# Kernel optimization log

Measured on AMD Instinct MI355X. Metric: run time of the kernel, lower is better.

Reference implementation:

```python
import jax, jax.numpy as jnp
import numpy as np

N_NODES = 100000
N_EDGES = 1600000
D_IN, D_HID, D_OUT = 64, 64, 2


def setup_inputs() -> dict:
    key = jax.random.key(0)
    k1, k2, k3, k4 = jax.random.split(key, 4)
    x = jax.random.normal(k1, (N_NODES, D_IN), dtype=jnp.float32)
    edge_index = jax.random.randint(k2, (2, N_EDGES), 0, N_NODES, dtype=jnp.int64)
    W1 = jax.random.normal(k3, (D_IN, D_HID), dtype=jnp.float32) * (1.0 / np.sqrt(D_IN))
    b1 = jnp.zeros((D_HID,), dtype=jnp.float32)
    W2 = jax.random.normal(k4, (D_HID, D_OUT), dtype=jnp.float32) * (1.0 / np.sqrt(D_HID))
    b2 = jnp.zeros((D_OUT,), dtype=jnp.float32)
    return {"x": x, "edge_index": edge_index, "W1": W1, "b1": b1, "W2": W2, "b2": b2}


def _gcn_norm(edge_index, num_nodes):
    # PyG GCNConv default: add self-loops, symmetric normalization D^-1/2 (A+I) D^-1/2
    loops = jnp.arange(num_nodes, dtype=edge_index.dtype)
    row = jnp.concatenate([edge_index[0], loops])  # source
    col = jnp.concatenate([edge_index[1], loops])  # destination
    deg = jax.ops.segment_sum(jnp.ones_like(col, dtype=jnp.float32), col, num_segments=num_nodes)
    dinv = jnp.where(deg > 0, jax.lax.rsqrt(deg), 0.0)
    norm = dinv[row] * dinv[col]  # [E + N]
    return row, col, norm


def _gcn_conv(x, W, b, row, col, norm, num_nodes):
    h = x @ W                              # [N, D_out] small GEMM first (PyG order)
    msg = h[row] * norm[:, None]           # gather + scale  [E+N, D_out]
    out = jax.ops.segment_sum(msg, col, num_segments=num_nodes)  # scatter-add
    return out + b


def reference(x, edge_index, W1, b1, W2, b2):
    n = x.shape[0]
    row, col, norm = _gcn_norm(edge_index, n)
    h = jax.nn.relu(_gcn_conv(x, W1, b1, row, col, norm, n))
    return _gcn_conv(h, W2, b2, row, col, norm, n)
```

## Files before the change

kernel.cpp:

```cpp
#include <hip/hip_runtime.h>


#define D_IN 64
#define NBBITS 10
#define NBK_PAD 128
#define BSTRIDE 16
#define PCH 8192
#define BCAP 16384
#define BCAPE 24576

__device__ __forceinline__ float b2f(unsigned short u) {
    unsigned v = ((unsigned)u) << 16;
    float f;
    __builtin_memcpy(&f, &v, 4);
    return f;
}
__device__ __forceinline__ unsigned short f2b(float f) {
    unsigned u;
    __builtin_memcpy(&u, &f, 4);
    u += 0x7FFFu + ((u >> 16) & 1u);
    return (unsigned short)(u >> 16);
}

__device__ __forceinline__ int edge_val(const int* __restrict__ p, int f64, long pos) {
    return f64 ? p[2 * pos] : p[pos];
}

__device__ __forceinline__ void acc8(float* a, uint4 rv, float wgt) {
    a[0] = fmaf(wgt, b2f((unsigned short)(rv.x & 0xFFFFu)), a[0]);
    a[1] = fmaf(wgt, b2f((unsigned short)(rv.x >> 16)), a[1]);
    a[2] = fmaf(wgt, b2f((unsigned short)(rv.y & 0xFFFFu)), a[2]);
    a[3] = fmaf(wgt, b2f((unsigned short)(rv.y >> 16)), a[3]);
    a[4] = fmaf(wgt, b2f((unsigned short)(rv.z & 0xFFFFu)), a[4]);
    a[5] = fmaf(wgt, b2f((unsigned short)(rv.z >> 16)), a[5]);
    a[6] = fmaf(wgt, b2f((unsigned short)(rv.w & 0xFFFFu)), a[6]);
    a[7] = fmaf(wgt, b2f((unsigned short)(rv.w >> 16)), a[7]);
}

__global__ __launch_bounds__(1024, 8) void k_part_gemm(
        const int* __restrict__ ep, int* __restrict__ bptr,
        unsigned* __restrict__ ebuf,
        const float* __restrict__ x, const float* __restrict__ W,
        unsigned short* __restrict__ H, int E, int N, int nPart) {
    __shared__ __align__(16) char smraw[51200];
    int tid = threadIdx.x;
    int lane = tid & 63;

    if (blockIdx.x < nPart) {
        int* hist  = (int*)smraw;
        int* lofs  = hist + NBK_PAD;
        int* gbase = lofs + NBK_PAD;
        int* fsh   = gbase + NBK_PAD;
        unsigned* stage = (unsigned*)(fsh + 4);

        if (tid < NBK_PAD) hist[tid] = 0;
        if (tid < 64) {
            int bad = 0;
            for (int i = tid; i < 1024; i += 64)
                if (ep[2 * i + 1] != 0) bad = 1;
            unsigned long long m = __ballot(bad);
            if (tid == 0) fsh[0] = (m == 0ull) ? 1 : 0;
        }
        __syncthreads();
        int f = fsh[0];
        long base = (long)blockIdx.x * PCH;
        long rem64 = (long)E - base;
        int nE = rem64 > PCH ? PCH : (int)rem64;
        int j0 = tid * 8;
        int nv = nE - j0;
        nv = nv < 0 ? 0 : (nv > 8 ? 8 : nv);
        unsigned cc[8], rr2[8];
        #pragma unroll
        for (int k = 0; k < 8; ++k) { cc[k] = 0; rr2[k] = 0; }
        bool fullv = (nv == 8);
        const uint4* p4 = (const uint4*)ep;
        if (f) {
            if (fullv && ((E & 1) == 0)) {
                size_t cb = ((size_t)E + (size_t)base + j0) >> 1;
                uint4 a0 = p4[cb + 0], a1 = p4[cb + 1];
                uint4 a2 = p4[cb + 2], a3 = p4[cb + 3];
                cc[0] = a0.x; cc[1] = a0.z; cc[2] = a1.x; cc[3] = a1.z;
                cc[4] = a2.x; cc[5] = a2.z; cc[6] = a3.x; cc[7] = a3.z;
            } else {
                for (int k = 0; k < 8; ++k)
                    if (k < nv) cc[k] = (unsigned)ep[2 * ((size_t)E + base + j0 + k)];
            }
        } else {
            if (fullv && ((E & 3) == 0)) {
                size_t cb = ((size_t)E + (size_t)base + j0) >> 2;
                uint4 a0 = p4[cb + 0], a1 = p4[cb + 1];
                cc[0] = a0.x; cc[1] = a0.y; cc[2] = a0.z; cc[3] = a0.w;
                cc[4] = a1.x; cc[5] = a1.y; cc[6] = a1.z; cc[7] = a1.w;
            } else {
                for (int k = 0; k < 8; ++k)
                    if (k < nv) cc[k] = (unsigned)ep[(size_t)E + base + j0 + k];
            }
        }
        #pragma unroll
        for (int k = 0; k < 8; ++k)
            if (k < nv) atomicAdd(&hist[cc[k] >> NBBITS], 1);
        if (f) {
            if (fullv && ((E & 1) == 0)) {
                size_t rb = ((size_t)base + j0) >> 1;
                uint4 b0 = p4[rb + 0], b1 = p4[rb + 1];
                uint4 b2 = p4[rb + 2], b3 = p4[rb + 3];
                rr2[0] = b0.x; rr2[1] = b0.z; rr2[2] = b1.x; rr2[3] = b1.z;
                rr2[4] = b2.x; rr2[5] = b2.z; rr2[6] = b3.x; rr2[7] = b3.z;
            } else {
                for (int k = 0; k < 8; ++k)
                    if (k < nv) rr2[k] = (unsigned)ep[2 * ((size_t)base + j0 + k)];
            }
        } else {
            if (fullv && ((E & 3) == 0)) {
                size_t rb = ((size_t)base + j0) >> 2;
                uint4 b0 = p4[rb + 0], b1 = p4[rb + 1];
                rr2[0] = b0.x; rr2[1] = b0.y; rr2[2] = b0.z; rr2[3] = b0.w;
                rr2[4] = b1.x; rr2[5] = b1.y; rr2[6] = b1.z; rr2[7] = b1.w;
            } else {
                for (int k = 0; k < 8; ++k)
                    if (k < nv) rr2[k] = (unsigned)ep[(size_t)base + j0 + k];
            }
        }
        __syncthreads();
        if (tid < NBK_PAD) {
            int c = hist[tid], s = c;
            #pragma unroll
            for (int off = 1; off < 64; off <<= 1) {
                int t2 = __shfl(s, lane - off);
                if (lane >= off) s += t2;
            }
            if (lane == 63) fsh[1 + (tid >> 6)] = s;
            lofs[tid] = s - c;
        }
        __syncthreads();
        if (tid >= 64 && tid < NBK_PAD) lofs[tid] += fsh[1];
        if (tid < NBK_PAD) hist[tid] = 0;
        __syncthreads();
        #pragma unroll
        for (int k = 0; k < 8; ++k) {
            if (k < nv) {
                unsigned c = cc[k];
                int b = c >> NBBITS;
                int pos = lofs[b] + atomicAdd(&hist[b], 1);
                stage[pos] = rr2[k] | ((c & ((1u << NBBITS) - 1)) << 17);
            }
        }
        __syncthreads();
        if (tid < NBK_PAD && hist[tid])
            gbase[tid] = atomicAdd(&bptr[tid * BSTRIDE], hist[tid]);
        __syncthreads();
        int wv = tid >> 6;
        for (int b = wv; b < NBK_PAD; b += 16) {
            int c = hist[b];
            if (c == 0) continue;
            int lo = lofs[b], go = gbase[b];
            unsigned* dst = ebuf + (size_t)b * BCAPE + go;
            for (int j = lane; j < c; j += 64) dst[j] = stage[lo + j];
        }
    } else {
        float* Ws = (float*)smraw;
        float* Xs = (float*)(smraw + 16384);
        int wv = tid >> 6;
        for (int i = tid; i < 64 * 64; i += 1024) Ws[i] = W[i];

        int bid = blockIdx.x - nPart;
        int ngb = gridDim.x - nPart;
        int ntiles = (N + 127) >> 7;
        for (int tile = bid; tile < ntiles; tile += ngb) {
            int rr = tid >> 4, c4 = tid & 15;
            int g0 = (tile << 7) + rr;
            int g1 = g0 + 64;
            float4 v0 = make_float4(0.f, 0.f, 0.f, 0.f);
            float4 v1 = make_float4(0.f, 0.f, 0.f, 0.f);
            if (g0 < N) v0 = *(const float4*)(x + (size_t)g0 * 64 + c4 * 4);
            if (g1 < N) v1 = *(const float4*)(x + (size_t)g1 * 64 + c4 * 4);
            __syncthreads();
            *(float4*)(&Xs[rr * 68 + c4 * 4]) = v0;
            *(float4*)(&Xs[(rr + 64) * 68 + c4 * 4]) = v1;
            __syncthreads();
            float acc[8];
            #pragma unroll
            for (int r = 0; r < 8; ++r) acc[r] = 0.f;
            int rbase = wv * 8;
            #pragma unroll 4
            for (int k4 = 0; k4 < 16; ++k4) {
                float w0 = Ws[(4 * k4 + 0) * 64 + lane];
                float w1 = Ws[(4 * k4 + 1) * 64 + lane];
                float w2 = Ws[(4 * k4 + 2) * 64 + lane];
                float w3 = Ws[(4 * k4 + 3) * 64 + lane];
                #pragma unroll
                for (int r = 0; r < 8; ++r) {
                    float4 xq = *(const float4*)(&Xs[(rbase + r) * 68 + k4 * 4]);
                    acc[r] = fmaf(xq.x, w0, acc[r]);
                    acc[r] = fmaf(xq.y, w1, acc[r]);
                    acc[r] = fmaf(xq.z, w2, acc[r]);
                    acc[r] = fmaf(xq.w, w3, acc[r]);
                }
            }
            int row0 = (tile << 7) + rbase;
            #pragma unroll
            for (int r = 0; r < 8; ++r) {
                int row = row0 + r;
                if (row < N) H[(size_t)row * 64 + lane] = f2b(acc[r]);
            }
        }
    }
}

__global__ __launch_bounds__(1024) void k_bucket(const unsigned* __restrict__ ebuf,
                                                 const int* __restrict__ bptr,
                                                 int* __restrict__ offs,
                                                 float* __restrict__ dinv,
                                                 int* __restrict__ srcA, int N, int E) {
    __shared__ int hist[1024], escan[1024], wsum[16];
    __shared__ int bco[NBK_PAD];
    __shared__ int stage[BCAP];
    int tid = threadIdx.x, b = blockIdx.x;
    int lane = tid & 63, wid = tid >> 6;
    hist[tid] = 0;
    if (tid < NBK_PAD) {
        int c = bptr[tid * BSTRIDE];
        int s = c;
        #pragma unroll
        for (int off = 1; off < 64; off <<= 1) {
            int t = __shfl(s, lane - off);
            if (lane >= off) s += t;
        }
        if (lane == 63) wsum[wid] = s;
        bco[tid] = s - c;
    }
    if (tid == 0 && b == 0) offs[N] = E;
    __syncthreads();
    if (tid >= 64 && tid < NBK_PAD) bco[tid] += wsum[0];
    __syncthreads();

    int rbase = b * BCAPE;
    int lo = bco[b];
    int m = bptr[b * BSTRIDE];
    for (int i = tid; i < m; i += 1024) {
        unsigned w = ebuf[rbase + i];
        atomicAdd(&hist[w >> 17], 1);
    }
    __syncthreads();
    int v = hist[tid];
    int s = v;
    #pragma unroll
    for (int off = 1; off < 64; off <<= 1) {
        int t = __shfl(s, lane - off);
        if (lane >= off) s += t;
    }
    if (lane == 63) wsum[wid] = s;
    __syncthreads();
    if (tid < 16) {
        int xv = wsum[tid];
        int ss = xv;
        #pragma unroll
        for (int off = 1; off < 16; off <<= 1) {
            int t = __shfl(ss, lane - off);
            if (lane >= off) ss += t;
        }
        wsum[tid] = ss - xv;
    }
    __syncthreads();
    int excl = s - v + wsum[wid];
    escan[tid] = excl;
    int g = (b << NBBITS) + tid;
    if (g < N) {
        offs[g] = lo + excl;
        dinv[g] = rsqrtf((float)(v + 1));
    }
    __syncthreads();
    for (int i = tid; i < m; i += 1024) {
        unsigned w = ebuf[rbase + i];
        int lc = w >> 17;
        int src = (int)(w & 0x1FFFFu);
        int sl = escan[lc] + atomicSub(&hist[lc], 1) - 1;
        if (sl < BCAP) stage[sl] = src;
        else srcA[lo + sl] = src;
    }
    __syncthreads();
    int mm = min(m, BCAP);
    for (int i = tid; i < mm; i += 1024) srcA[lo + i] = stage[i];
}

__global__ void k_agg1(const unsigned short* __restrict__ H1,
                       const int* __restrict__ srcA,
                       const float* __restrict__ dinv, const int* __restrict__ offs,
                       const float* __restrict__ b1, const float* __restrict__ W2,
                       float* __restrict__ Z, int N) {
    int wid = (blockIdx.x * blockDim.x + threadIdx.x) >> 6;
    int lane = threadIdx.x & 63;
    int g = lane >> 3, s = lane & 7;
    int n = wid * 8 + g;
    bool nvalid = (n < N);
    int nn = nvalid ? n : 0;
    float dn = dinv[nn];
    int base = offs[nn];
    int cnt = nvalid ? (offs[nn + 1] - base) : 0;
    int cm = cnt;
    #pragma unroll
    for (int off = 8; off <= 32; off <<= 1) cm = max(cm, __shfl_xor(cm, off));
    const uint4* H4 = (const uint4*)H1;
    uint4 rs = H4[(size_t)nn * 8 + s];
    float4 b1a = *(const float4*)(b1 + s * 8);
    float4 b1b = *(const float4*)(b1 + s * 8 + 4);
    const float4* w2p = (const float4*)(W2 + s * 16);
    float4 q0 = w2p[0], q1 = w2p[1], q2 = w2p[2], q3 = w2p[3];
    float a[8];
    #pragma unroll
    for (int k = 0; k < 8; ++k) a[k] = 0.f;
    int gb = g << 3;
    int sv = 0; float wl = 0.f;
    if (s < cnt) { sv = srcA[base + s]; wl = dinv[sv]; }
    for (int j0 = 0; j0 < cm; j0 += 8) {
        int svn = 0; float wln = 0.f;
        int jn = j0 + 8;
        if (jn + s < cnt) { svn = srcA[base + jn + s]; wln = dinv[svn]; }
        int   s0 = __shfl(sv, gb + 0), s1 = __shfl(sv, gb + 1);
        int   s2 = __shfl(sv, gb + 2), s3 = __shfl(sv, gb + 3);
        int   s4 = __shfl(sv, gb + 4), s5 = __shfl(sv, gb + 5);
        int   s6 = __shfl(sv, gb + 6), s7 = __shfl(sv, gb + 7);
        float w0 = __shfl(wl, gb + 0), w1 = __shfl(wl, gb + 1);
        float w2 = __shfl(wl, gb + 2), w3 = __shfl(wl, gb + 3);
        float w4 = __shfl(wl, gb + 4), w5 = __shfl(wl, gb + 5);
        float w6 = __shfl(wl, gb + 6), w7 = __shfl(wl, gb + 7);
        uint4 r0 = H4[(size_t)s0 * 8 + s];
        uint4 r1 = H4[(size_t)s1 * 8 + s];
        uint4 r2 = H4[(size_t)s2 * 8 + s];
        uint4 r3 = H4[(size_t)s3 * 8 + s];
        uint4 r4 = H4[(size_t)s4 * 8 + s];
        uint4 r5 = H4[(size_t)s5 * 8 + s];
        uint4 r6 = H4[(size_t)s6 * 8 + s];
        uint4 r7 = H4[(size_t)s7 * 8 + s];
        acc8(a, r0, w0); acc8(a, r1, w1); acc8(a, r2, w2); acc8(a, r3, w3);
        acc8(a, r4, w4); acc8(a, r5, w5); acc8(a, r6, w6); acc8(a, r7, w7);
        sv = svn; wl = wln;
    }
    acc8(a, rs, dn);
    float h0 = fmaxf(dn * a[0] + b1a.x, 0.f);
    float h1 = fmaxf(dn * a[1] + b1a.y, 0.f);
    float h2 = fmaxf(dn * a[2] + b1a.z, 0.f);
    float h3 = fmaxf(dn * a[3] + b1a.w, 0.f);
    float h4 = fmaxf(dn * a[4] + b1b.x, 0.f);
    float h5 = fmaxf(dn * a[5] + b1b.y, 0.f);
    float h6 = fmaxf(dn * a[6] + b1b.z, 0.f);
    float h7 = fmaxf(dn * a[7] + b1b.w, 0.f);
    float p0 = h0 * q0.x + h1 * q0.z + h2 * q1.x + h3 * q1.z
             + h4 * q2.x + h5 * q2.z + h6 * q3.x + h7 * q3.z;
    float p1 = h0 * q0.y + h1 * q0.w + h2 * q1.y + h3 * q1.w
             + h4 * q2.y + h5 * q2.w + h6 * q3.y + h7 * q3.w;
    #pragma unroll
    for (int off = 1; off < 8; off <<= 1) {
        p0 += __shfl_xor(p0, off);
        p1 += __shfl_xor(p1, off);
    }
    if (s == 0 && nvalid) { Z[n * 2 + 0] = p0; Z[n * 2 + 1] = p1; }
}

__global__ void k_agg2(const float* __restrict__ Z, const int* __restrict__ srcA,
                       const float* __restrict__ dinv, const int* __restrict__ offs,
                       const float* __restrict__ b2, float* __restrict__ out, int N) {
    int t = blockIdx.x * blockDim.x + threadIdx.x;
    int lane = threadIdx.x & 63;
    int n = (t >> 6) * 4 + (lane >> 4);
    int sl = lane & 15;
    if (n >= N) return;
    int base = offs[n];
    int cnt = offs[n + 1] - base;
    float a0 = 0.f, a1 = 0.f;
    const float2* Z2 = (const float2*)Z;
    for (int i = sl; i < cnt; i += 16) {
        int src = srcA[base + i];
        float w = dinv[src];
        float2 zv = Z2[src];
        a0 += w * zv.x;
        a1 += w * zv.y;
    }
    #pragma unroll
    for (int off = 8; off > 0; off >>= 1) {
        a0 += __shfl_xor(a0, off);
        a1 += __shfl_xor(a1, off);
    }
    if (sl == 0) {
        float dn = dinv[n];
        float2 zs = Z2[n];
        out[n * 2 + 0] = dn * (a0 + dn * zs.x) + b2[0];
        out[n * 2 + 1] = dn * (a1 + dn * zs.y) + b2[1];
    }
}

extern "C" void kernel_launch(void* const* d_in, const int* in_sizes, int n_in,
                              void* d_out, int out_size, void* d_ws, size_t ws_size,
                              hipStream_t stream) {
    const float* x  = (const float*)d_in[0];
    const int*   ep = (const int*)d_in[1];
    const float* W1 = (const float*)d_in[2];
    const float* b1 = (const float*)d_in[3];
    const float* W2 = (const float*)d_in[4];
    const float* b2 = (const float*)d_in[5];
    float* out = (float*)d_out;

    const int N = in_sizes[0] / D_IN;
    const int E = in_sizes[1] / 2;

    char* ws = (char*)d_ws;
    size_t o = 0;
    auto alloc = [&](size_t bytes) {
        size_t r = o;
        o = (o + bytes + 255) & ~(size_t)255;
        return r;
    };
    int*            bptr  = (int*)           (ws + alloc((size_t)NBK_PAD * BSTRIDE * 4));
    float*          dinv  = (float*)         (ws + alloc((size_t)N * 4));
    int*            offs  = (int*)           (ws + alloc((size_t)(N + 1) * 4));
    unsigned*       ebuf  = (unsigned*)      (ws + alloc((size_t)NBK_PAD * BCAPE * 4));
    int*            srcA  = (int*)           (ws + alloc((size_t)E * 4));
    unsigned short* H1    = (unsigned short*)(ws + alloc((size_t)N * 64 * 2));
    float*          Z     = (float*)         (ws + alloc((size_t)N * 2 * 4));

    const int nbk = (N + (1 << NBBITS) - 1) >> NBBITS;
    const int nPart = (E + PCH - 1) / PCH;
    int nGemm = 512 - nPart;
    if (nGemm < 64) nGemm = 64;

    (void)hipMemsetAsync(bptr, 0, (size_t)NBK_PAD * BSTRIDE * sizeof(int), stream);
    k_part_gemm<<<nPart + nGemm, 1024, 0, stream>>>(ep, bptr, ebuf, x, W1, H1, E, N, nPart);
    k_bucket<<<nbk, 1024, 0, stream>>>(ebuf, bptr, offs, dinv, srcA, N, E);
    int nwav = (N + 7) / 8;
    k_agg1<<<(nwav + 3) / 4, 256, 0, stream>>>(H1, srcA, dinv, offs, b1, W2, Z, N);
    k_agg2<<<(N + 15) / 16, 256, 0, stream>>>(Z, srcA, dinv, offs, b2, out, N);
}
```

Baseline: 104.6 us.

## Fuse bucket sort with layer-1 aggregation using finer buckets and global degree counts

Buckets shrink from 1024 to 256 destination nodes, giving 512 buckets, and the per-bucket CSR build is merged with the first aggregation kernel. Each block now sorts its bucket's edges and aggregates its nodes directly from shared-memory staged sources, which removes one kernel launch and a global round trip for srcA. Source-node normalisation needs degrees of nodes in other buckets, so the partition kernel now keeps a global per-node degree array via atomics. This adds 1.6M global atomics and an rsqrt per edge, and leaves only 4 small blocks of nodes per 1024-thread block for aggregation work, which may limit parallelism.

After: 164.7 us. 1.57x slower.

```diff
diff --git a/kernel.cpp b/kernel.cpp
--- a/kernel.cpp
+++ b/kernel.cpp
@@ -2,12 +2,11 @@
 
 
 #define D_IN 64
-#define NBBITS 10
-#define NBK_PAD 128
+#define NBBITS 8
+#define NBK_PAD 512
 #define BSTRIDE 16
 #define PCH 8192
-#define BCAP 16384
-#define BCAPE 24576
+#define SCAP 5120
 
 __device__ __forceinline__ float b2f(unsigned short u) {
     unsigned v = ((unsigned)u) << 16;
@@ -20,10 +19,6 @@
     __builtin_memcpy(&u, &f, 4);
     u += 0x7FFFu + ((u >> 16) & 1u);
     return (unsigned short)(u >> 16);
-}
-
-__device__ __forceinline__ int edge_val(const int* __restrict__ p, int f64, long pos) {
-    return f64 ? p[2 * pos] : p[pos];
 }
 
 __device__ __forceinline__ void acc8(float* a, uint4 rv, float wgt) {
@@ -39,7 +34,7 @@
 
 __global__ __launch_bounds__(1024, 8) void k_part_gemm(
         const int* __restrict__ ep, int* __restrict__ bptr,
-        unsigned* __restrict__ ebuf,
+        int* __restrict__ deg, unsigned* __restrict__ ebuf,
         const float* __restrict__ x, const float* __restrict__ W,
         unsigned short* __restrict__ H, int E, int N, int nPart) {
     __shared__ __align__(16) char smraw[51200];
@@ -51,7 +46,7 @@
         int* lofs  = hist + NBK_PAD;
         int* gbase = lofs + NBK_PAD;
         int* fsh   = gbase + NBK_PAD;
-        unsigned* stage = (unsigned*)(fsh + 4);
+        unsigned* stage = (unsigned*)(fsh + 16);
 
         if (tid < NBK_PAD) hist[tid] = 0;
         if (tid < 64) {
@@ -98,12 +93,15 @@
         }
         #pragma unroll
         for (int k = 0; k < 8; ++k)
-            if (k < nv) atomicAdd(&hist[cc[k] >> NBBITS], 1);
+            if (k < nv) {
+                atomicAdd(&hist[cc[k] >> NBBITS], 1);
+                atomicAdd(&deg[cc[k]], 1);
+            }
         if (f) {
             if (fullv && ((E & 1) == 0)) {
-                size_t rb = ((size_t)base + j0) >> 1;
-                uint4 b0 = p4[rb + 0], b1 = p4[rb + 1];
-                uint4 b2 = p4[rb + 2], b3 = p4[rb + 3];
+                size_t rbb = ((size_t)base + j0) >> 1;
+                uint4 b0 = p4[rbb + 0], b1 = p4[rbb + 1];
+                uint4 b2 = p4[rbb + 2], b3 = p4[rbb + 3];
                 rr2[0] = b0.x; rr2[1] = b0.z; rr2[2] = b1.x; rr2[3] = b1.z;
                 rr2[4] = b2.x; rr2[5] = b2.z; rr2[6] = b3.x; rr2[7] = b3.z;
             } else {
@@ -112,8 +110,8 @@
             }
         } else {
             if (fullv && ((E & 3) == 0)) {
-                size_t rb = ((size_t)base + j0) >> 2;
-                uint4 b0 = p4[rb + 0], b1 = p4[rb + 1];
+                size_t rbb = ((size_t)base + j0) >> 2;
+                uint4 b0 = p4[rbb + 0], b1 = p4[rbb + 1];
                 rr2[0] = b0.x; rr2[1] = b0.y; rr2[2] = b0.z; rr2[3] = b0.w;
                 rr2[4] = b1.x; rr2[5] = b1.y; rr2[6] = b1.z; rr2[7] = b1.w;
             } else {
@@ -133,16 +131,22 @@
             lofs[tid] = s - c;
         }
         __syncthreads();
-        if (tid >= 64 && tid < NBK_PAD) lofs[tid] += fsh[1];
-        if (tid < NBK_PAD) hist[tid] = 0;
+        if (tid < NBK_PAD) {
+            int w8 = tid >> 6, add = 0;
+            #pragma unroll
+            for (int q = 0; q < 8; ++q)
+                if (q < w8) add += fsh[1 + q];
+            lofs[tid] += add;
+            hist[tid] = 0;
+        }
         __syncthreads();
         #pragma unroll
         for (int k = 0; k < 8; ++k) {
             if (k < nv) {
                 unsigned c = cc[k];
-                int b = c >> NBBITS;
-                int pos = lofs[b] + atomicAdd(&hist[b], 1);
-                stage[pos] = rr2[k] | ((c & ((1u << NBBITS) - 1)) << 17);
+                int bb = c >> NBBITS;
+                int pos = lofs[bb] + atomicAdd(&hist[bb], 1);
+                stage[pos] = rr2[k] | ((c & 255u) << 17);
             }
         }
         __syncthreads();
@@ -150,12 +154,12 @@
             gbase[tid] = atomicAdd(&bptr[tid * BSTRIDE], hist[tid]);
         __syncthreads();
         int wv = tid >> 6;
-        for (int b = wv; b < NBK_PAD; b += 16) {
-            int c = hist[b];
+        for (int bb = wv; bb < NBK_PAD; bb += 16) {
+            int c = hist[bb];
             if (c == 0) continue;
-            int lo = lofs[b], go = gbase[b];
-            unsigned* dst = ebuf + (size_t)b * BCAPE + go;
-            for (int j = lane; j < c; j += 64) dst[j] = stage[lo + j];
+            int lo2 = lofs[bb], go = gbase[bb];
+            unsigned* dst = ebuf + (size_t)bb * SCAP + go;
+            for (int j = lane; j < c; j += 64) dst[j] = stage[lo2 + j];
         }
     } else {
         float* Ws = (float*)smraw;
@@ -207,154 +211,145 @@
     }
 }
 
-__global__ __launch_bounds__(1024) void k_bucket(const unsigned* __restrict__ ebuf,
-                                                 const int* __restrict__ bptr,
-                                                 int* __restrict__ offs,
-                                                 float* __restrict__ dinv,
-                                                 int* __restrict__ srcA, int N, int E) {
-    __shared__ int hist[1024], escan[1024], wsum[16];
-    __shared__ int bco[NBK_PAD];
-    __shared__ int stage[BCAP];
+__global__ __launch_bounds__(1024, 4) void k_bucket_agg(
+        const unsigned* __restrict__ ebuf, const int* __restrict__ bptr,
+        const int* __restrict__ deg,
+        int* __restrict__ offs, float* __restrict__ dinv,
+        int* __restrict__ srcA,
+        const unsigned short* __restrict__ H1,
+        const float* __restrict__ b1, const float* __restrict__ W2,
+        float* __restrict__ Z, int N, int E) {
+    __shared__ int cntS[256];
+    __shared__ int escan[257];
+    __shared__ float dinvsh[256];
+    __shared__ int wsum[16];
+    __shared__ int loSh;
+    __shared__ int stage[SCAP];
     int tid = threadIdx.x, b = blockIdx.x;
     int lane = tid & 63, wid = tid >> 6;
-    hist[tid] = 0;
-    if (tid < NBK_PAD) {
-        int c = bptr[tid * BSTRIDE];
-        int s = c;
-        #pragma unroll
-        for (int off = 1; off < 64; off <<= 1) {
-            int t = __shfl(s, lane - off);
-            if (lane >= off) s += t;
-        }
-        if (lane == 63) wsum[wid] = s;
-        bco[tid] = s - c;
-    }
-    if (tid == 0 && b == 0) offs[N] = E;
-    __syncthreads();
-    if (tid >= 64 && tid < NBK_PAD) bco[tid] += wsum[0];
-    __syncthreads();
-
-    int rbase = b * BCAPE;
-    int lo = bco[b];
-    int m = bptr[b * BSTRIDE];
-    for (int i = tid; i < m; i += 1024) {
-        unsigned w = ebuf[rbase + i];
-        atomicAdd(&hist[w >> 17], 1);
-    }
-    __syncthreads();
-    int v = hist[tid];
-    int s = v;
-    #pragma unroll
-    for (int off = 1; off < 64; off <<= 1) {
-        int t = __shfl(s, lane - off);
-        if (lane >= off) s += t;
-    }
-    if (lane == 63) wsum[wid] = s;
-    __syncthreads();
-    if (tid < 16) {
-        int xv = wsum[tid];
-        int ss = xv;
-        #pragma unroll
-        for (int off = 1; off < 16; off <<= 1) {
-            int t = __shfl(ss, lane - off);
-            if (lane >= off) ss += t;
-        }
-        wsum[tid] = ss - xv;
-    }
-    __syncthreads();
-    int excl = s - v + wsum[wid];
-    escan[tid] = excl;
-    int g = (b << NBBITS) + tid;
-    if (g < N) {
-        offs[g] = lo + excl;
-        dinv[g] = rsqrtf((float)(v + 1));
-    }
-    __syncthreads();
-    for (int i = tid; i < m; i += 1024) {
-        unsigned w = ebuf[rbase + i];
-        int lc = w >> 17;
-        int src = (int)(w & 0x1FFFFu);
-        int sl = escan[lc] + atomicSub(&hist[lc], 1) - 1;
-        if (sl < BCAP) stage[sl] = src;
-        else srcA[lo + sl] = src;
-    }
-    __syncthreads();
-    int mm = min(m, BCAP);
-    for (int i = tid; i < mm; i += 1024) srcA[lo + i] = stage[i];
-}
-
-__global__ void k_agg1(const unsigned short* __restrict__ H1,
-                       const int* __restrict__ srcA,
-                       const float* __restrict__ dinv, const int* __restrict__ offs,
-                       const float* __restrict__ b1, const float* __restrict__ W2,
-                       float* __restrict__ Z, int N) {
-    int wid = (blockIdx.x * blockDim.x + threadIdx.x) >> 6;
-    int lane = threadIdx.x & 63;
-    int g = lane >> 3, s = lane & 7;
-    int n = wid * 8 + g;
-    bool nvalid = (n < N);
-    int nn = nvalid ? n : 0;
-    float dn = dinv[nn];
-    int base = offs[nn];
-    int cnt = nvalid ? (offs[nn + 1] - base) : 0;
-    int cm = cnt;
-    #pragma unroll
-    for (int off = 8; off <= 32; off <<= 1) cm = max(cm, __shfl_xor(cm, off));
-    const uint4* H4 = (const uint4*)H1;
-    uint4 rs = H4[(size_t)nn * 8 + s];
+    int s = tid & 7, gb = lane & 56;
     float4 b1a = *(const float4*)(b1 + s * 8);
     float4 b1b = *(const float4*)(b1 + s * 8 + 4);
     const float4* w2p = (const float4*)(W2 + s * 16);
     float4 q0 = w2p[0], q1 = w2p[1], q2 = w2p[2], q3 = w2p[3];
-    float a[8];
+
+    if (tid < 256) cntS[tid] = 0;
+    int cb = 0;
+    if (tid < NBK_PAD && tid < b) cb = bptr[tid * BSTRIDE];
     #pragma unroll
-    for (int k = 0; k < 8; ++k) a[k] = 0.f;
-    int gb = g << 3;
-    int sv = 0; float wl = 0.f;
-    if (s < cnt) { sv = srcA[base + s]; wl = dinv[sv]; }
-    for (int j0 = 0; j0 < cm; j0 += 8) {
-        int svn = 0; float wln = 0.f;
-        int jn = j0 + 8;
-        if (jn + s < cnt) { svn = srcA[base + jn + s]; wln = dinv[svn]; }
-        int   s0 = __shfl(sv, gb + 0), s1 = __shfl(sv, gb + 1);
-        int   s2 = __shfl(sv, gb + 2), s3 = __shfl(sv, gb + 3);
-        int   s4 = __shfl(sv, gb + 4), s5 = __shfl(sv, gb + 5);
-        int   s6 = __shfl(sv, gb + 6), s7 = __shfl(sv, gb + 7);
-        float w0 = __shfl(wl, gb + 0), w1 = __shfl(wl, gb + 1);
-        float w2 = __shfl(wl, gb + 2), w3 = __shfl(wl, gb + 3);
-        float w4 = __shfl(wl, gb + 4), w5 = __shfl(wl, gb + 5);
-        float w6 = __shfl(wl, gb + 6), w7 = __shfl(wl, gb + 7);
-        uint4 r0 = H4[(size_t)s0 * 8 + s];
-        uint4 r1 = H4[(size_t)s1 * 8 + s];
-        uint4 r2 = H4[(size_t)s2 * 8 + s];
-        uint4 r3 = H4[(size_t)s3 * 8 + s];
-        uint4 r4 = H4[(size_t)s4 * 8 + s];
-        uint4 r5 = H4[(size_t)s5 * 8 + s];
-        uint4 r6 = H4[(size_t)s6 * 8 + s];
-        uint4 r7 = H4[(size_t)s7 * 8 + s];
-        acc8(a, r0, w0); acc8(a, r1, w1); acc8(a, r2, w2); acc8(a, r3, w3);
-        acc8(a, r4, w4); acc8(a, r5, w5); acc8(a, r6, w6); acc8(a, r7, w7);
-        sv = svn; wl = wln;
-    }
-    acc8(a, rs, dn);
-    float h0 = fmaxf(dn * a[0] + b1a.x, 0.f);
-    float h1 = fmaxf(dn * a[1] + b1a.y, 0.f);
-    float h2 = fmaxf(dn * a[2] + b1a.z, 0.f);
-    float h3 = fmaxf(dn * a[3] + b1a.w, 0.f);
-    float h4 = fmaxf(dn * a[4] + b1b.x, 0.f);
-    float h5 = fmaxf(dn * a[5] + b1b.y, 0.f);
-    float h6 = fmaxf(dn * a[6] + b1b.z, 0.f);
-    float h7 = fmaxf(dn * a[7] + b1b.w, 0.f);
-    float p0 = h0 * q0.x + h1 * q0.z + h2 * q1.x + h3 * q1.z
-             + h4 * q2.x + h5 * q2.z + h6 * q3.x + h7 * q3.z;
-    float p1 = h0 * q0.y + h1 * q0.w + h2 * q1.y + h3 * q1.w
-             + h4 * q2.y + h5 * q2.w + h6 * q3.y + h7 * q3.w;
-    #pragma unroll
-    for (int off = 1; off < 8; off <<= 1) {
-        p0 += __shfl_xor(p0, off);
-        p1 += __shfl_xor(p1, off);
-    }
-    if (s == 0 && nvalid) { Z[n * 2 + 0] = p0; Z[n * 2 + 1] = p1; }
+    for (int off = 32; off > 0; off >>= 1) cb += __shfl_xor(cb, off);
+    if (lane == 0) wsum[wid] = cb;
+    __syncthreads();
+    if (tid == 0) {
+        int t = 0;
+        #pragma unroll
+        for (int q = 0; q < 16; ++q) t += wsum[q];
+        loSh = t;
+    }
+    __syncthreads();
+    int lo = loSh;
+    int m = bptr[b * BSTRIDE];
+    size_t rb = (size_t)b * SCAP;
+    for (int i = tid; i < m; i += 1024)
+        atomicAdd(&cntS[ebuf[rb + i] >> 17], 1);
+    __syncthreads();
+    if (tid < 256) {
+        int v = cntS[tid], ss = v;
+        #pragma unroll
+        for (int off = 1; off < 64; off <<= 1) {
+            int t2 = __shfl(ss, lane - off);
+            if (lane >= off) ss += t2;
+        }
+        if (lane == 63) wsum[tid >> 6] = ss;
+        escan[tid] = ss - v;
+    }
+    if (tid == 0) escan[256] = m;
+    __syncthreads();
+    if (tid < 256) {
+        int w4 = tid >> 6, add = 0;
+        #pragma unroll
+        for (int q = 0; q < 4; ++q)
+            if (q < w4) add += wsum[q];
+        int ex = escan[tid] + add;
+        escan[tid] = ex;
+        float dn = rsqrtf((float)(cntS[tid] + 1));
+        dinvsh[tid] = dn;
+        int g = (b << NBBITS) + tid;
+        if (g < N) { offs[g] = lo + ex; dinv[g] = dn; }
+    }
+    if (tid == 0 && b == 0) offs[N] = E;
+    __syncthreads();
+    for (int i = tid; i < m; i += 1024) {
+        unsigned w = ebuf[rb + i];
+        int lc = w >> 17;
+        int src = (int)(w & 0x1FFFFu);
+        int sl = escan[lc] + atomicSub(&cntS[lc], 1) - 1;
+        if (sl < SCAP) stage[sl] = src;
+        else srcA[lo + sl] = src;
+    }
+    __syncthreads();
+    int mm = min(m, SCAP);
+    for (int i = tid; i < mm; i += 1024) srcA[lo + i] = stage[i];
+    const uint4* H4 = (const uint4*)H1;
+    int grp = tid >> 3;
+    for (int r = 0; r < 2; ++r) {
+        int loc = grp + (r << 7);
+        int n = (b << NBBITS) + loc;
+        if (n >= N) break;
+        int start = escan[loc];
+        int cnt = escan[loc + 1] - start;
+        float dn = dinvsh[loc];
+        float a[8];
+        #pragma unroll
+        for (int k = 0; k < 8; ++k) a[k] = 0.f;
+        for (int j = 0; j < cnt; j += 8) {
+            int e = j + s;
+            int sv = 0; float wl = 0.f;
+            if (e < cnt) {
+                int sl = start + e;
+                sv = (sl < SCAP) ? stage[sl] : srcA[lo + sl];
+                wl = rsqrtf((float)(deg[sv] + 1));
+            }
+            int   s0 = __shfl(sv, gb + 0), s1 = __shfl(sv, gb + 1);
+            int   s2 = __shfl(sv, gb + 2), s3 = __shfl(sv, gb + 3);
+            int   s4 = __shfl(sv, gb + 4), s5 = __shfl(sv, gb + 5);
+            int   s6 = __shfl(sv, gb + 6), s7 = __shfl(sv, gb + 7);
+            float w0 = __shfl(wl, gb + 0), w1 = __shfl(wl, gb + 1);
+            float w2 = __shfl(wl, gb + 2), w3 = __shfl(wl, gb + 3);
+            float w4 = __shfl(wl, gb + 4), w5 = __shfl(wl, gb + 5);
+            float w6 = __shfl(wl, gb + 6), w7 = __shfl(wl, gb + 7);
+            uint4 r0 = H4[(size_t)s0 * 8 + s];
+            uint4 r1 = H4[(size_t)s1 * 8 + s];
+            uint4 r2 = H4[(size_t)s2 * 8 + s];
+            uint4 r3 = H4[(size_t)s3 * 8 + s];
+            uint4 r4 = H4[(size_t)s4 * 8 + s];
+            uint4 r5 = H4[(size_t)s5 * 8 + s];
+            uint4 r6 = H4[(size_t)s6 * 8 + s];
+            uint4 r7 = H4[(size_t)s7 * 8 + s];
+            acc8(a, r0, w0); acc8(a, r1, w1); acc8(a, r2, w2); acc8(a, r3, w3);
+            acc8(a, r4, w4); acc8(a, r5, w5); acc8(a, r6, w6); acc8(a, r7, w7);
+        }
+        uint4 rs = H4[(size_t)n * 8 + s];
+        acc8(a, rs, dn);
+        float h0 = fmaxf(dn * a[0] + b1a.x, 0.f);
+        float h1 = fmaxf(dn * a[1] + b1a.y, 0.f);
+        float h2 = fmaxf(dn * a[2] + b1a.z, 0.f);
+        float h3 = fmaxf(dn * a[3] + b1a.w, 0.f);
+        float h4 = fmaxf(dn * a[4] + b1b.x, 0.f);
+        float h5 = fmaxf(dn * a[5] + b1b.y, 0.f);
+        float h6 = fmaxf(dn * a[6] + b1b.z, 0.f);
+        float h7 = fmaxf(dn * a[7] + b1b.w, 0.f);
+        float p0 = h0 * q0.x + h1 * q0.z + h2 * q1.x + h3 * q1.z
+                 + h4 * q2.x + h5 * q2.z + h6 * q3.x + h7 * q3.z;
+        float p1 = h0 * q0.y + h1 * q0.w + h2 * q1.y + h3 * q1.w
+                 + h4 * q2.y + h5 * q2.w + h6 * q3.y + h7 * q3.w;
+        #pragma unroll
+        for (int off = 1; off < 8; off <<= 1) {
+            p0 += __shfl_xor(p0, off);
+            p1 += __shfl_xor(p1, off);
+        }
+        if (s == 0) { Z[n * 2 + 0] = p0; Z[n * 2 + 1] = p1; }
+    }
 }
 
 __global__ void k_agg2(const float* __restrict__ Z, const int* __restrict__ srcA,
@@ -411,9 +406,10 @@
         return r;
     };
     int*            bptr  = (int*)           (ws + alloc((size_t)NBK_PAD * BSTRIDE * 4));
+    int*            deg   = (int*)           (ws + alloc((size_t)N * 4));
     float*          dinv  = (float*)         (ws + alloc((size_t)N * 4));
     int*            offs  = (int*)           (ws + alloc((size_t)(N + 1) * 4));
-    unsigned*       ebuf  = (unsigned*)      (ws + alloc((size_t)NBK_PAD * BCAPE * 4));
+    unsigned*       ebuf  = (unsigned*)      (ws + alloc((size_t)NBK_PAD * SCAP * 4));
     int*            srcA  = (int*)           (ws + alloc((size_t)E * 4));
     unsigned short* H1    = (unsigned short*)(ws + alloc((size_t)N * 64 * 2));
     float*          Z     = (float*)         (ws + alloc((size_t)N * 2 * 4));
@@ -423,10 +419,10 @@
     int nGemm = 512 - nPart;
     if (nGemm < 64) nGemm = 64;
 
-    (void)hipMemsetAsync(bptr, 0, (size_t)NBK_PAD * BSTRIDE * sizeof(int), stream);
-    k_part_gemm<<<nPart + nGemm, 1024, 0, stream>>>(ep, bptr, ebuf, x, W1, H1, E, N, nPart);
-    k_bucket<<<nbk, 1024, 0, stream>>>(ebuf, bptr, offs, dinv, srcA, N, E);
-    int nwav = (N + 7) / 8;
-    k_agg1<<<(nwav + 3) / 4, 256, 0, stream>>>(H1, srcA, dinv, offs, b1, W2, Z, N);
+    (void)hipMemsetAsync(bptr, 0,
+            (size_t)NBK_PAD * BSTRIDE * 4 + (size_t)N * 4, stream);
+    k_part_gemm<<<nPart + nGemm, 1024, 0, stream>>>(ep, bptr, deg, ebuf, x, W1, H1, E, N, nPart);
+    k_bucket_agg<<<nbk, 1024, 0, stream>>>(ebuf, bptr, deg, offs, dinv, srcA,
+                                           H1, b1, W2, Z, N, E);
     k_agg2<<<(N + 15) / 16, 256, 0, stream>>>(Z, srcA, dinv, offs, b2, out, N);
 }
```

## Use bf16 MFMA for first-layer GEMM and per-wave histograms in partitioning

Applied to the files above, without the earlier changes.

The GEMM blocks now convert W to a transposed bf16 tile and compute x@W1 with 16x16x32 bf16 MFMA instructions, one 16-row tile per wave, replacing the scalar FMA loop over shared-memory tiles. The partition blocks switch from a single shared histogram to per-wave histograms with per-wave prefix offsets, which cuts contention on shared-memory atomics during counting and scatter. The grid shrinks from 512 to 256 total blocks and launch bounds drop to 4 blocks per CU. Rounding x to bf16 before the multiply slightly lowers GEMM precision.

New measurement: 97.11 us. -7.1%, faster.

```diff
diff --git a/kernel.cpp b/kernel.cpp
--- a/kernel.cpp
+++ b/kernel.cpp
@@ -9,6 +9,9 @@
 #define BCAP 16384
 #define BCAPE 24576
 
+typedef __attribute__((ext_vector_type(8))) short bf16x8;
+typedef __attribute__((ext_vector_type(4))) float f32x4;
+
 __device__ __forceinline__ float b2f(unsigned short u) {
     unsigned v = ((unsigned)u) << 16;
     float f;
@@ -20,10 +23,6 @@
     __builtin_memcpy(&u, &f, 4);
     u += 0x7FFFu + ((u >> 16) & 1u);
     return (unsigned short)(u >> 16);
-}
-
-__device__ __forceinline__ int edge_val(const int* __restrict__ p, int f64, long pos) {
-    return f64 ? p[2 * pos] : p[pos];
 }
 
 __device__ __forceinline__ void acc8(float* a, uint4 rv, float wgt) {
@@ -37,23 +36,25 @@
     a[7] = fmaf(wgt, b2f((unsigned short)(rv.w >> 16)), a[7]);
 }
 
-__global__ __launch_bounds__(1024, 8) void k_part_gemm(
+__global__ __launch_bounds__(1024, 4) void k_part_gemm(
         const int* __restrict__ ep, int* __restrict__ bptr,
         unsigned* __restrict__ ebuf,
         const float* __restrict__ x, const float* __restrict__ W,
-        unsigned short* __restrict__ H, int E, int N, int nPart) {
-    __shared__ __align__(16) char smraw[51200];
+        unsigned short* __restrict__ H, int E, int N, int nPart, int nGemm) {
+    __shared__ __align__(16) char smraw[43520];
     int tid = threadIdx.x;
     int lane = tid & 63;
+    int wv = tid >> 6;
 
     if (blockIdx.x < nPart) {
-        int* hist  = (int*)smraw;
-        int* lofs  = hist + NBK_PAD;
-        int* gbase = lofs + NBK_PAD;
+        int* whist = (int*)smraw;
+        int* lofs  = whist + 16 * NBK_PAD;
+        int* hcnt  = lofs + NBK_PAD;
+        int* gbase = hcnt + NBK_PAD;
         int* fsh   = gbase + NBK_PAD;
-        unsigned* stage = (unsigned*)(fsh + 4);
-
-        if (tid < NBK_PAD) hist[tid] = 0;
+        unsigned* stage = (unsigned*)(fsh + 8);
+
+        for (int i = tid; i < 16 * NBK_PAD; i += 1024) whist[i] = 0;
         if (tid < 64) {
             int bad = 0;
             for (int i = tid; i < 1024; i += 64)
@@ -96,14 +97,15 @@
                     if (k < nv) cc[k] = (unsigned)ep[(size_t)E + base + j0 + k];
             }
         }
+        int* myh = whist + wv * NBK_PAD;
         #pragma unroll
         for (int k = 0; k < 8; ++k)
-            if (k < nv) atomicAdd(&hist[cc[k] >> NBBITS], 1);
+            if (k < nv) atomicAdd(&myh[cc[k] >> NBBITS], 1);
         if (f) {
             if (fullv && ((E & 1) == 0)) {
-                size_t rb = ((size_t)base + j0) >> 1;
-                uint4 b0 = p4[rb + 0], b1 = p4[rb + 1];
-                uint4 b2 = p4[rb + 2], b3 = p4[rb + 3];
+                size_t rbb = ((size_t)base + j0) >> 1;
+                uint4 b0 = p4[rbb + 0], b1 = p4[rbb + 1];
+                uint4 b2 = p4[rbb + 2], b3 = p4[rbb + 3];
                 rr2[0] = b0.x; rr2[1] = b0.z; rr2[2] = b1.x; rr2[3] = b1.z;
                 rr2[4] = b2.x; rr2[5] = b2.z; rr2[6] = b3.x; rr2[7] = b3.z;
             } else {
@@ -112,8 +114,8 @@
             }
         } else {
             if (fullv && ((E & 3) == 0)) {
-                size_t rb = ((size_t)base + j0) >> 2;
-                uint4 b0 = p4[rb + 0], b1 = p4[rb + 1];
+                size_t rbb = ((size_t)base + j0) >> 2;
+                uint4 b0 = p4[rbb + 0], b1 = p4[rbb + 1];
                 rr2[0] = b0.x; rr2[1] = b0.y; rr2[2] = b0.z; rr2[3] = b0.w;
                 rr2[4] = b1.x; rr2[5] = b1.y; rr2[6] = b1.z; rr2[7] = b1.w;
             } else {
@@ -123,86 +125,99 @@
         }
         __syncthreads();
         if (tid < NBK_PAD) {
-            int c = hist[tid], s = c;
+            int run = 0;
+            #pragma unroll
+            for (int w = 0; w < 16; ++w) {
+                int v = whist[w * NBK_PAD + tid];
+                whist[w * NBK_PAD + tid] = run;
+                run += v;
+            }
+            hcnt[tid] = run;
+            int s = run;
             #pragma unroll
             for (int off = 1; off < 64; off <<= 1) {
                 int t2 = __shfl(s, lane - off);
                 if (lane >= off) s += t2;
             }
             if (lane == 63) fsh[1 + (tid >> 6)] = s;
-            lofs[tid] = s - c;
+            lofs[tid] = s - run;
         }
         __syncthreads();
         if (tid >= 64 && tid < NBK_PAD) lofs[tid] += fsh[1];
-        if (tid < NBK_PAD) hist[tid] = 0;
+        __syncthreads();
+        for (int i = tid; i < 16 * NBK_PAD; i += 1024)
+            whist[i] += lofs[i & (NBK_PAD - 1)];
         __syncthreads();
         #pragma unroll
         for (int k = 0; k < 8; ++k) {
             if (k < nv) {
                 unsigned c = cc[k];
                 int b = c >> NBBITS;
-                int pos = lofs[b] + atomicAdd(&hist[b], 1);
+                int pos = atomicAdd(&myh[b], 1);
                 stage[pos] = rr2[k] | ((c & ((1u << NBBITS) - 1)) << 17);
             }
         }
         __syncthreads();
-        if (tid < NBK_PAD && hist[tid])
-            gbase[tid] = atomicAdd(&bptr[tid * BSTRIDE], hist[tid]);
-        __syncthreads();
-        int wv = tid >> 6;
+        if (tid < NBK_PAD && hcnt[tid])
+            gbase[tid] = atomicAdd(&bptr[tid * BSTRIDE], hcnt[tid]);
+        __syncthreads();
         for (int b = wv; b < NBK_PAD; b += 16) {
-            int c = hist[b];
+            int c = hcnt[b];
             if (c == 0) continue;
             int lo = lofs[b], go = gbase[b];
             unsigned* dst = ebuf + (size_t)b * BCAPE + go;
             for (int j = lane; j < c; j += 64) dst[j] = stage[lo + j];
         }
     } else {
-        float* Ws = (float*)smraw;
-        float* Xs = (float*)(smraw + 16384);
-        int wv = tid >> 6;
-        for (int i = tid; i < 64 * 64; i += 1024) Ws[i] = W[i];
-
-        int bid = blockIdx.x - nPart;
-        int ngb = gridDim.x - nPart;
-        int ntiles = (N + 127) >> 7;
-        for (int tile = bid; tile < ntiles; tile += ngb) {
-            int rr = tid >> 4, c4 = tid & 15;
-            int g0 = (tile << 7) + rr;
-            int g1 = g0 + 64;
-            float4 v0 = make_float4(0.f, 0.f, 0.f, 0.f);
-            float4 v1 = make_float4(0.f, 0.f, 0.f, 0.f);
-            if (g0 < N) v0 = *(const float4*)(x + (size_t)g0 * 64 + c4 * 4);
-            if (g1 < N) v1 = *(const float4*)(x + (size_t)g1 * 64 + c4 * 4);
-            __syncthreads();
-            *(float4*)(&Xs[rr * 68 + c4 * 4]) = v0;
-            *(float4*)(&Xs[(rr + 64) * 68 + c4 * 4]) = v1;
-            __syncthreads();
-            float acc[8];
-            #pragma unroll
-            for (int r = 0; r < 8; ++r) acc[r] = 0.f;
-            int rbase = wv * 8;
-            #pragma unroll 4
-            for (int k4 = 0; k4 < 16; ++k4) {
-                float w0 = Ws[(4 * k4 + 0) * 64 + lane];
-                float w1 = Ws[(4 * k4 + 1) * 64 + lane];
-                float w2 = Ws[(4 * k4 + 2) * 64 + lane];
-                float w3 = Ws[(4 * k4 + 3) * 64 + lane];
+        unsigned short* Wt = (unsigned short*)smraw;
+        for (int i = tid; i < 64 * 64; i += 1024) {
+            int c = i & 63, k = i >> 6;
+            Wt[c * 64 + k] = f2b(W[k * 64 + c]);
+        }
+        __syncthreads();
+        int lm = lane & 15, lk = lane >> 4;
+        bf16x8 bfrag[4][2];
+        #pragma unroll
+        for (int ct = 0; ct < 4; ++ct)
+            #pragma unroll
+            for (int ks = 0; ks < 2; ++ks) {
+                int col = ct * 16 + lm;
+                int kb = ks * 32 + lk * 8;
+                bfrag[ct][ks] = *(const bf16x8*)(Wt + col * 64 + kb);
+            }
+        int gwid = (blockIdx.x - nPart) * 16 + wv;
+        int wstride = nGemm * 16;
+        int ntiles = (N + 15) >> 4;
+        for (int tile = gwid; tile < ntiles; tile += wstride) {
+            int rbase = tile << 4;
+            int arow = rbase + lm;
+            const float* xr = x + (size_t)(arow < N ? arow : N - 1) * 64;
+            bf16x8 afrag[2];
+            #pragma unroll
+            for (int ks = 0; ks < 2; ++ks) {
+                float4 u0 = *(const float4*)(xr + ks * 32 + lk * 8);
+                float4 u1 = *(const float4*)(xr + ks * 32 + lk * 8 + 4);
+                afrag[ks][0] = (short)f2b(u0.x); afrag[ks][1] = (short)f2b(u0.y);
+                afrag[ks][2] = (short)f2b(u0.z); afrag[ks][3] = (short)f2b(u0.w);
+                afrag[ks][4] = (short)f2b(u1.x); afrag[ks][5] = (short)f2b(u1.y);
+                afrag[ks][6] = (short)f2b(u1.z); afrag[ks][7] = (short)f2b(u1.w);
+            }
+            f32x4 acc[4] = {{0.f, 0.f, 0.f, 0.f}, {0.f, 0.f, 0.f, 0.f},
+                            {0.f, 0.f, 0.f, 0.f}, {0.f, 0.f, 0.f, 0.f}};
+            #pragma unroll
+            for (int ks = 0; ks < 2; ++ks)
                 #pragma unroll
-                for (int r = 0; r < 8; ++r) {
-                    float4 xq = *(const float4*)(&Xs[(rbase + r) * 68 + k4 * 4]);
-                    acc[r] = fmaf(xq.x, w0, acc[r]);
-                    acc[r] = fmaf(xq.y, w1, acc[r]);
-                    acc[r] = fmaf(xq.z, w2, acc[r]);
-                    acc[r] = fmaf(xq.w, w3, acc[r]);
+                for (int ct = 0; ct < 4; ++ct)
+                    acc[ct] = __builtin_amdgcn_mfma_f32_16x16x32_bf16(
+                        afrag[ks], bfrag[ct][ks], acc[ct], 0, 0, 0);
+            #pragma unroll
+            for (int ct = 0; ct < 4; ++ct)
+                #pragma unroll
+                for (int j = 0; j < 4; ++j) {
+                    int row = rbase + lk * 4 + j;
+                    if (row < N)
+                        H[(size_t)row * 64 + ct * 16 + lm] = f2b(acc[ct][j]);
                 }
-            }
-            int row0 = (tile << 7) + rbase;
-            #pragma unroll
-            for (int r = 0; r < 8; ++r) {
-                int row = row0 + r;
-                if (row < N) H[(size_t)row * 64 + lane] = f2b(acc[r]);
-            }
         }
     }
 }
@@ -420,11 +435,12 @@
 
     const int nbk = (N + (1 << NBBITS) - 1) >> NBBITS;
     const int nPart = (E + PCH - 1) / PCH;
-    int nGemm = 512 - nPart;
-    if (nGemm < 64) nGemm = 64;
+    int nGemm = 256 - nPart;
+    if (nGemm < 32) nGemm = 32;
 
     (void)hipMemsetAsync(bptr, 0, (size_t)NBK_PAD * BSTRIDE * sizeof(int), stream);
-    k_part_gemm<<<nPart + nGemm, 1024, 0, stream>>>(ep, bptr, ebuf, x, W1, H1, E, N, nPart);
+    k_part_gemm<<<nPart + nGemm, 1024, 0, stream>>>(ep, bptr, ebuf, x, W1, H1,
+                                                    E, N, nPart, nGemm);
     k_bucket<<<nbk, 1024, 0, stream>>>(ebuf, bptr, offs, dinv, srcA, N, E);
     int nwav = (N + 7) / 8;
     k_agg1<<<(nwav + 3) / 4, 256, 0, stream>>>(H1, srcA, dinv, offs, b1, W2, Z, N);
```
